# Kernel optimization log

Measured on AMD Instinct MI355X. Metric: run time of the kernel, lower is better.

The kernel has to match this reference:

```python
import jax, jax.numpy as jnp
import numpy as np

B, T, DIM, H, L = 16, 4096, 256, 128, 3  # hidden = dim // 2, 3 bidirectional layers


def setup_inputs() -> dict:
    key = jax.random.key(0)
    kx, ki, kh, kb = jax.random.split(key, 4)
    x = jax.random.normal(kx, (B, T, DIM), dtype=jnp.float32)
    # stacked params: [layer, direction(0=fwd,1=bwd), ...]; gates packed as (r, z, n)
    Wi = jax.random.normal(ki, (L, 2, DIM, 3 * H), dtype=jnp.float32) / np.sqrt(DIM).astype(np.float32)
    Wh = jax.random.normal(kh, (L, 2, H, 3 * H), dtype=jnp.float32) / np.sqrt(H).astype(np.float32)
    bh = jax.random.normal(kb, (L, 2, 3 * H), dtype=jnp.float32) * 0.01
    return {"x": x, "Wi": Wi, "Wh": Wh, "bh": bh}


def _gru_dir(x, Wi, Wh, bh, reverse):
    """Run a GRU over time; x [B,T,D] -> h sequence [B,T,H].

    flax nnx.GRUCell math: input denses have no bias, hidden denses have bias;
    n-gate hidden contribution (incl. its bias) is gated by r.
    """
    # precompute all input-side gate projections in one big GEMM (efficient)
    xg = jnp.einsum('btd,dk->btk', x, Wi)  # [B,T,3H]
    Whr, Whz, Whn = jnp.split(Wh, 3, axis=1)
    bhr, bhz, bhn = jnp.split(bh, 3)

    def step(h, xg_t):
        xr, xz, xn = jnp.split(xg_t, 3, axis=-1)
        r = jax.nn.sigmoid(xr + h @ Whr + bhr)
        z = jax.nn.sigmoid(xz + h @ Whz + bhz)
        n = jnp.tanh(xn + r * (h @ Whn + bhn))
        h_new = (1.0 - z) * n + z * h
        return h_new, h_new

    h0 = jnp.zeros((x.shape[0], Whr.shape[0]), x.dtype)
    _, ys = jax.lax.scan(step, h0, jnp.swapaxes(xg, 0, 1), reverse=reverse)
    return jnp.swapaxes(ys, 0, 1)  # [B,T,H], time-aligned with input (keep_order)


def reference(x, Wi, Wh, bh):
    n_layers = Wi.shape[0]
    for l in range(n_layers):
        fwd = _gru_dir(x, Wi[l, 0], Wh[l, 0], bh[l, 0], reverse=False)
        bwd = _gru_dir(x, Wi[l, 1], Wh[l, 1], bh[l, 1], reverse=True)
        x = jnp.concatenate([fwd, bwd], axis=-1)  # [B,T,2H]=[B,T,DIM]
    return x
```

## Files before the change

kernel.cpp:

```cpp
#include <hip/hip_runtime.h>

#define BB 16
#define TT 4096
#define DD 256
#define HH 128
#define G3 384
#define MM (BB*TT)

typedef unsigned short u16;
typedef unsigned int u32;
typedef __attribute__((ext_vector_type(8))) short short8;
typedef __attribute__((ext_vector_type(4))) float f32x4;
typedef __attribute__((ext_vector_type(2))) unsigned int u32x2;
typedef __attribute__((ext_vector_type(4))) unsigned int u32x4;

__device__ __forceinline__ float bf2f(u16 u) {
    return __uint_as_float(((u32)u) << 16);
}
__device__ __forceinline__ u16 f2bf(float f) {
    u32 u = __float_as_uint(f);
    u32 lsb = (u >> 16) & 1u;
    u += 0x7fffu + lsb;
    return (u16)(u >> 16);
}

__device__ __forceinline__ u32 cvt_pk2(float x, float y) {
    u32 pk;
    asm("v_cvt_pk_bf16_f32 %0, %1, %2" : "=v"(pk) : "v"(x), "v"(y));
    return pk;
}
__device__ __forceinline__ u32 cvt_bf16(float f) {
    u32 pk;
    asm("v_cvt_pk_bf16_f32 %0, %1, %2" : "=v"(pk) : "v"(f), "v"(f));
    return pk;
}
__device__ __forceinline__ void cvt2_hilo(float x, float y, u32& hi, u32& lo) {
    u32 h = cvt_pk2(x, y);
    float rx = x - __uint_as_float(h << 16);
    float ry = y - __uint_as_float(h & 0xffff0000u);
    hi = h;
    lo = cvt_pk2(rx, ry);
}

#define GBM 128
#define GBN 128
#define GBK 32
#define APAD 40

__global__ __launch_bounds__(256, 2) void gemm_in(const float* __restrict__ X,
                                                  const float* __restrict__ Wi,
                                                  float* __restrict__ XG) {
    __shared__ __align__(16) u16 Ahi[GBM][APAD];
    __shared__ __align__(16) u16 Alo[GBM][APAD];
    __shared__ __align__(16) u16 Bhi[GBN][APAD];
    __shared__ __align__(16) u16 Blo[GBN][APAD];

    const int tid = threadIdx.x;
    const int m0  = blockIdx.y * GBM;
    const int gc0 = blockIdx.x * GBN;
    const int dir = (gc0 >= G3) ? 1 : 0;
    const int n0  = gc0 - dir * G3;
    const float* Wd = Wi + (size_t)dir * DD * G3;

    const int lane = tid & 63;
    const int wv   = tid >> 6;
    const int wr   = wv >> 1;
    const int wc   = wv & 1;
    const int q    = lane >> 4;
    const int c    = lane & 15;

    f32x4 acc[4][4];
    #pragma unroll
    for (int i = 0; i < 4; ++i)
        #pragma unroll
        for (int j = 0; j < 4; ++j) acc[i][j] = (f32x4){0.f, 0.f, 0.f, 0.f};

    const int bn  = tid & 127;
    const int bkh = (tid >> 7) * 16;

    for (int k0 = 0; k0 < DD; k0 += GBK) {
        #pragma unroll
        for (int p = 0; p < 4; ++p) {
            int idx = tid + p * 256;
            int row = idx >> 3;
            int k4  = (idx & 7) * 4;
            float4 v = *(const float4*)(X + (size_t)(m0 + row) * DD + k0 + k4);
            u32 h01, l01, h23, l23;
            cvt2_hilo(v.x, v.y, h01, l01);
            cvt2_hilo(v.z, v.w, h23, l23);
            *(u32x2*)(&Ahi[row][k4]) = (u32x2){h01, h23};
            *(u32x2*)(&Alo[row][k4]) = (u32x2){l01, l23};
        }
        {
            float bv[16];
            #pragma unroll
            for (int j = 0; j < 16; ++j)
                bv[j] = Wd[(size_t)(k0 + bkh + j) * G3 + n0 + bn];
            u32 h[8], l[8];
            #pragma unroll
            for (int j = 0; j < 8; ++j)
                cvt2_hilo(bv[2 * j], bv[2 * j + 1], h[j], l[j]);
            *(u32x4*)(&Bhi[bn][bkh + 0]) = (u32x4){h[0], h[1], h[2], h[3]};
            *(u32x4*)(&Bhi[bn][bkh + 8]) = (u32x4){h[4], h[5], h[6], h[7]};
            *(u32x4*)(&Blo[bn][bkh + 0]) = (u32x4){l[0], l[1], l[2], l[3]};
            *(u32x4*)(&Blo[bn][bkh + 8]) = (u32x4){l[4], l[5], l[6], l[7]};
        }
        __syncthreads();
        short8 afh[4], afl[4], bfh[4], bfl[4];
        #pragma unroll
        for (int i = 0; i < 4; ++i) {
            afh[i] = *(const short8*)(&Ahi[wr * 64 + i * 16 + c][q * 8]);
            afl[i] = *(const short8*)(&Alo[wr * 64 + i * 16 + c][q * 8]);
            bfh[i] = *(const short8*)(&Bhi[wc * 64 + i * 16 + c][q * 8]);
            bfl[i] = *(const short8*)(&Blo[wc * 64 + i * 16 + c][q * 8]);
        }
        #pragma unroll
        for (int i = 0; i < 4; ++i)
            #pragma unroll
            for (int j = 0; j < 4; ++j) {
                acc[i][j] = __builtin_amdgcn_mfma_f32_16x16x32_bf16(afh[i], bfh[j], acc[i][j], 0, 0, 0);
                acc[i][j] = __builtin_amdgcn_mfma_f32_16x16x32_bf16(afh[i], bfl[j], acc[i][j], 0, 0, 0);
                acc[i][j] = __builtin_amdgcn_mfma_f32_16x16x32_bf16(afl[i], bfh[j], acc[i][j], 0, 0, 0);
            }
        __syncthreads();
    }
    #pragma unroll
    for (int i = 0; i < 4; ++i) {
        #pragma unroll
        for (int j = 0; j < 4; ++j) {
            const int n = n0 + wc * 64 + j * 16 + c;
            #pragma unroll
            for (int r = 0; r < 4; ++r) {
                const int m = m0 + wr * 64 + i * 16 + q * 4 + r;
                XG[((size_t)dir * MM + m) * G3 + n] = acc[i][j][r];
            }
        }
    }
}

__device__ __forceinline__ float fast_sigmoid(float x) {
    float e = __expf(-x);
    return __builtin_amdgcn_rcpf(1.f + e);
}
__device__ __forceinline__ float fast_tanh(float x) {
    float e = __expf(2.f * x);
    return 1.f - 2.f * __builtin_amdgcn_rcpf(1.f + e);
}

__device__ __forceinline__ float permswap_add(float g) {
    u32 gu = __float_as_uint(g);
    u32x2 r = __builtin_amdgcn_permlane32_swap(gu, gu, false, false);
    return __uint_as_float(r[0]) + __uint_as_float(r[1]);
}

struct XG3 { float r, z, n; };
__device__ __forceinline__ XG3 load3(const float* p) {
    XG3 v;
    v.r = p[0];
    v.z = p[128];
    v.n = p[256];
    return v;
}

#define HLO_OFF (2 * HH + 32)

__global__ __launch_bounds__(512, 1) void gru_rec(const float* __restrict__ XG,
                                                  const float* __restrict__ Wh,
                                                  const float* __restrict__ bh,
                                                  float* __restrict__ Xout) {
    const int wg   = blockIdx.x;
    const int dir  = wg & 1;
    const int b    = wg >> 1;
    const int tid  = threadIdx.x;
    const int lane = tid & 63;
    const int wave = tid >> 6;
    const int q    = lane >> 4;
    const int c    = lane & 15;
    const int hcol = wave * 16 + c;

    __shared__ __align__(16) u16 hbuf[HLO_OFF + 2 * HH];

    short8 bfr[3][4];
    {
        const float* W = Wh + (size_t)dir * HH * G3;
        #pragma unroll
        for (int g = 0; g < 3; ++g) {
            const int n = g * 128 + hcol;
            #pragma unroll
            for (int ch = 0; ch < 4; ++ch) {
                short8 vh;
                #pragma unroll
                for (int j = 0; j < 8; ++j) {
                    int k = ch * 32 + q * 8 + j;
                    vh[j] = (short)f2bf(W[(size_t)k * G3 + n]);
                }
                bfr[g][ch] = vh;
            }
        }
    }
    float hb[3];
    #pragma unroll
    for (int g = 0; g < 3; ++g) hb[g] = 0.5f * bh[dir * G3 + g * 128 + hcol];

    short8 a[4];
    #pragma unroll
    for (int ch = 0; ch < 4; ++ch)
        #pragma unroll
        for (int j = 0; j < 8; ++j) a[ch][j] = 0;
    float ho = 0.f;

    f32x4 accR = {0.f, 0.f, 0.f, 0.f};
    f32x4 accZ = {0.f, 0.f, 0.f, 0.f};
    f32x4 accN = {0.f, 0.f, 0.f, 0.f};

    const int t0    = dir ? (TT - 1) : 0;
    const int gstep = dir ? -G3 : G3;
    const int ostep = dir ? -DD : DD;

    const float* xp = XG + ((size_t)dir * MM + (size_t)b * TT + t0) * G3 + hcol;
    float* op = Xout + ((size_t)b * TT + t0) * DD + dir * HH + hcol;

    const u16* hrd = hbuf + ((c < 8) ? 0 : HLO_OFF) + q * 8;
    u16* hw_hi = hbuf + hcol;
    u16* hw_lo = hbuf + HLO_OFF + hcol;

    XG3 x0 = load3(xp);
    XG3 x1 = load3(xp + gstep);
    XG3 x2 = load3(xp + 2 * gstep);
    XG3 x3 = load3(xp + 3 * gstep);
    const float* xpf = xp + 4 * gstep;

#define SUBSTEP(S, XV, PK)                                                     \
    {                                                                          \
            \
        float xr = XV.r, xz = XV.z, xn = XV.n;                                 \
        if (t + (S) + 4 < TT) { XV = load3(xpf + (PK) * gstep); }              \
                  \
        accR[0] = __builtin_fmaf(0.5f, xr, hb[0]);                             \
        accZ[0] = __builtin_fmaf(0.5f, xz, hb[1]);                             \
        accN[0] = hb[2];                                                       \
                                   \
        _Pragma("unroll")                                                      \
        for (int ch = 0; ch < 4; ++ch) {                                       \
            accR = __builtin_amdgcn_mfma_f32_16x16x32_bf16(a[ch], bfr[0][ch], accR, 0, 0, 0); \
            accZ = __builtin_amdgcn_mfma_f32_16x16x32_bf16(a[ch], bfr[1][ch], accZ, 0, 0, 0); \
            accN = __builtin_amdgcn_mfma_f32_16x16x32_bf16(a[ch], bfr[2][ch], accN, 0, 0, 0); \
        }                                                                      \
        float pr = permswap_add(accR[0]);                                      \
        float pz = permswap_add(accZ[0]);                                      \
        float pm = permswap_add(accN[0]);                                      \
        float rg = fast_sigmoid(pr);                                           \
        float zg = fast_sigmoid(pz);                                           \
        float ng = fast_tanh(xn + rg * pm);                                    \
        float hn = (1.f - zg) * ng + zg * ho;                                  \
        ho = hn;                                                               \
                                 \
        u32 pk_hi = cvt_bf16(hn);                                              \
        float lo_f = hn - __uint_as_float(pk_hi << 16);                        \
        u32 pk_lo = cvt_bf16(lo_f);                                            \
        const int pb = ((S) + 1) & 1;                                          \
        if (q == 0) {                                                          \
            op[(S) * ostep] = hn;                                              \
            hw_hi[pb * HH]  = (u16)pk_hi;                                      \
        } else if (q == 1) {                                                   \
            hw_lo[pb * HH]  = (u16)pk_lo;                                      \
        }                                                                      \
        asm volatile("s_waitcnt lgkmcnt(0)\n\ts_barrier" ::: "memory");        \
        if (t + (S) + 1 < TT) {                                                \
            a[0] = *(const short8*)(hrd + pb * HH + 0);                        \
            a[1] = *(const short8*)(hrd + pb * HH + 32);                       \
            a[2] = *(const short8*)(hrd + pb * HH + 64);                       \
            a[3] = *(const short8*)(hrd + pb * HH + 96);                       \
        }                                                                      \
    }

    for (int t = 0; t < TT; t += 4) {
        SUBSTEP(0, x0, 0)
        SUBSTEP(1, x1, 1)
        xpf += 2 * gstep;
        SUBSTEP(2, x2, 0)
        SUBSTEP(3, x3, 1)
        xpf += 2 * gstep;
        op += 4 * ostep;
    }
#undef SUBSTEP
}

extern "C" void kernel_launch(void* const* d_in, const int* in_sizes, int n_in,
                              void* d_out, int out_size, void* d_ws, size_t ws_size,
                              hipStream_t stream) {
    const float* x  = (const float*)d_in[0];
    const float* Wi = (const float*)d_in[1];
    const float* Wh = (const float*)d_in[2];
    const float* bh = (const float*)d_in[3];
    float* out = (float*)d_out;

    float* XG = (float*)d_ws;

    for (int l = 0; l < 3; ++l) {
        const float* in  = (l == 0) ? x : out;
        const float* Wil = Wi + (size_t)l * 2 * DD * G3;
        const float* Whl = Wh + (size_t)l * 2 * HH * G3;
        const float* bhl = bh + (size_t)l * 2 * G3;

        gemm_in<<<dim3(6, MM / GBM), 256, 0, stream>>>(in, Wil, XG);
        gru_rec<<<32, 512, 0, stream>>>(XG, Whl, bhl, out);
    }
}
```

Before: 5.667 ms.

## Halve recurrent workgroup to 4 waves, each computing two 16-column tiles

```diff
diff --git a/kernel.cpp b/kernel.cpp
--- a/kernel.cpp
+++ b/kernel.cpp
@@ -153,18 +153,18 @@
     return __uint_as_float(r[0]) + __uint_as_float(r[1]);
 }
 
-struct XG3 { float r, z, n; };
-__device__ __forceinline__ XG3 load3(const float* p) {
-    XG3 v;
-    v.r = p[0];
-    v.z = p[128];
-    v.n = p[256];
+struct XG6 { float r0, r1, z0, z1, n0, n1; };
+__device__ __forceinline__ XG6 load6(const float* p) {
+    XG6 v;
+    v.r0 = p[0];   v.r1 = p[16];
+    v.z0 = p[128]; v.z1 = p[144];
+    v.n0 = p[256]; v.n1 = p[272];
     return v;
 }
 
 #define HLO_OFF (2 * HH + 32)
 
-__global__ __launch_bounds__(512, 1) void gru_rec(const float* __restrict__ XG,
+__global__ __launch_bounds__(256, 1) void gru_rec(const float* __restrict__ XG,
                                                   const float* __restrict__ Wh,
                                                   const float* __restrict__ bh,
                                                   float* __restrict__ Xout) {
@@ -176,94 +176,124 @@
     const int wave = tid >> 6;
     const int q    = lane >> 4;
     const int c    = lane & 15;
-    const int hcol = wave * 16 + c;
+    const int col0 = wave * 32 + c;
 
     __shared__ __align__(16) u16 hbuf[HLO_OFF + 2 * HH];
 
-    short8 bfr[3][4];
+    short8 bfr[3][2][4];
     {
         const float* W = Wh + (size_t)dir * HH * G3;
         #pragma unroll
-        for (int g = 0; g < 3; ++g) {
-            const int n = g * 128 + hcol;
-            #pragma unroll
-            for (int ch = 0; ch < 4; ++ch) {
-                short8 vh;
+        for (int g = 0; g < 3; ++g)
+            #pragma unroll
+            for (int ti = 0; ti < 2; ++ti) {
+                const int n = g * 128 + wave * 32 + ti * 16 + c;
                 #pragma unroll
-                for (int j = 0; j < 8; ++j) {
-                    int k = ch * 32 + q * 8 + j;
-                    vh[j] = (short)f2bf(W[(size_t)k * G3 + n]);
+                for (int ch = 0; ch < 4; ++ch) {
+                    short8 vh;
+                    #pragma unroll
+                    for (int j = 0; j < 8; ++j) {
+                        int k = ch * 32 + q * 8 + j;
+                        vh[j] = (short)f2bf(W[(size_t)k * G3 + n]);
+                    }
+                    bfr[g][ti][ch] = vh;
                 }
-                bfr[g][ch] = vh;
             }
-        }
-    }
-    float hb[3];
+    }
+    float hb[3][2];
     #pragma unroll
-    for (int g = 0; g < 3; ++g) hb[g] = 0.5f * bh[dir * G3 + g * 128 + hcol];
+    for (int g = 0; g < 3; ++g)
+        #pragma unroll
+        for (int ti = 0; ti < 2; ++ti)
+            hb[g][ti] = 0.5f * bh[dir * G3 + g * 128 + wave * 32 + ti * 16 + c];
 
     short8 a[4];
     #pragma unroll
     for (int ch = 0; ch < 4; ++ch)
         #pragma unroll
         for (int j = 0; j < 8; ++j) a[ch][j] = 0;
-    float ho = 0.f;
-
-    f32x4 accR = {0.f, 0.f, 0.f, 0.f};
-    f32x4 accZ = {0.f, 0.f, 0.f, 0.f};
-    f32x4 accN = {0.f, 0.f, 0.f, 0.f};
+    float ho0 = 0.f, ho1 = 0.f;
+
+    f32x4 aR0 = {0,0,0,0}, aZ0 = {0,0,0,0}, aN0 = {0,0,0,0};
+    f32x4 aR1 = {0,0,0,0}, aZ1 = {0,0,0,0}, aN1 = {0,0,0,0};
 
     const int t0    = dir ? (TT - 1) : 0;
     const int gstep = dir ? -G3 : G3;
     const int ostep = dir ? -DD : DD;
 
-    const float* xp = XG + ((size_t)dir * MM + (size_t)b * TT + t0) * G3 + hcol;
-    float* op = Xout + ((size_t)b * TT + t0) * DD + dir * HH + hcol;
+    const float* xp = XG + ((size_t)dir * MM + (size_t)b * TT + t0) * G3 + col0;
+    float* op = Xout + ((size_t)b * TT + t0) * DD + dir * HH + col0;
 
     const u16* hrd = hbuf + ((c < 8) ? 0 : HLO_OFF) + q * 8;
-    u16* hw_hi = hbuf + hcol;
-    u16* hw_lo = hbuf + HLO_OFF + hcol;
-
-    XG3 x0 = load3(xp);
-    XG3 x1 = load3(xp + gstep);
-    XG3 x2 = load3(xp + 2 * gstep);
-    XG3 x3 = load3(xp + 3 * gstep);
+    u16* hw_hi = hbuf + col0;
+    u16* hw_lo = hbuf + HLO_OFF + col0;
+
+    XG6 x0 = load6(xp);
+    XG6 x1 = load6(xp + gstep);
+    XG6 x2 = load6(xp + 2 * gstep);
+    XG6 x3 = load6(xp + 3 * gstep);
     const float* xpf = xp + 4 * gstep;
 
 #define SUBSTEP(S, XV, PK)                                                     \
     {                                                                          \
             \
-        float xr = XV.r, xz = XV.z, xn = XV.n;                                 \
-        if (t + (S) + 4 < TT) { XV = load3(xpf + (PK) * gstep); }              \
+        float xr0 = XV.r0, xr1 = XV.r1, xz0 = XV.z0, xz1 = XV.z1;              \
+        float xn0 = XV.n0, xn1 = XV.n1;                                        \
+        if (t + (S) + 4 < TT) { XV = load6(xpf + (PK) * gstep); }              \
                   \
-        accR[0] = __builtin_fmaf(0.5f, xr, hb[0]);                             \
-        accZ[0] = __builtin_fmaf(0.5f, xz, hb[1]);                             \
-        accN[0] = hb[2];                                                       \
-                                   \
+        aR0[0] = __builtin_fmaf(0.5f, xr0, hb[0][0]);                          \
+        aZ0[0] = __builtin_fmaf(0.5f, xz0, hb[1][0]);                          \
+        aN0[0] = hb[2][0];                                                     \
+        aR1[0] = __builtin_fmaf(0.5f, xr1, hb[0][1]);                          \
+        aZ1[0] = __builtin_fmaf(0.5f, xz1, hb[1][1]);                          \
+        aN1[0] = hb[2][1];                                                     \
+                       \
         _Pragma("unroll")                                                      \
         for (int ch = 0; ch < 4; ++ch) {                                       \
-            accR = __builtin_amdgcn_mfma_f32_16x16x32_bf16(a[ch], bfr[0][ch], accR, 0, 0, 0); \
-            accZ = __builtin_amdgcn_mfma_f32_16x16x32_bf16(a[ch], bfr[1][ch], accZ, 0, 0, 0); \
-            accN = __builtin_amdgcn_mfma_f32_16x16x32_bf16(a[ch], bfr[2][ch], accN, 0, 0, 0); \
-        }                                                                      \
-        float pr = permswap_add(accR[0]);                                      \
-        float pz = permswap_add(accZ[0]);                                      \
-        float pm = permswap_add(accN[0]);                                      \
-        float rg = fast_sigmoid(pr);                                           \
-        float zg = fast_sigmoid(pz);                                           \
-        float ng = fast_tanh(xn + rg * pm);                                    \
-        float hn = (1.f - zg) * ng + zg * ho;                                  \
-        ho = hn;                                                               \
-                                 \
-        u32 pk_hi = cvt_bf16(hn);                                              \
-        float lo_f = hn - __uint_as_float(pk_hi << 16);                        \
-        u32 pk_lo = cvt_bf16(lo_f);                                            \
+            aR0 = __builtin_amdgcn_mfma_f32_16x16x32_bf16(a[ch], bfr[0][0][ch], aR0, 0, 0, 0); \
+            aZ0 = __builtin_amdgcn_mfma_f32_16x16x32_bf16(a[ch], bfr[1][0][ch], aZ0, 0, 0, 0); \
+            aN0 = __builtin_amdgcn_mfma_f32_16x16x32_bf16(a[ch], bfr[2][0][ch], aN0, 0, 0, 0); \
+            aR1 = __builtin_amdgcn_mfma_f32_16x16x32_bf16(a[ch], bfr[0][1][ch], aR1, 0, 0, 0); \
+            aZ1 = __builtin_amdgcn_mfma_f32_16x16x32_bf16(a[ch], bfr[1][1][ch], aZ1, 0, 0, 0); \
+            aN1 = __builtin_amdgcn_mfma_f32_16x16x32_bf16(a[ch], bfr[2][1][ch], aN1, 0, 0, 0); \
+        }                                                                      \
+        float hn0, hn1;                                                        \
+        {                                                                      \
+            float pr = permswap_add(aR0[0]);                                   \
+            float pz = permswap_add(aZ0[0]);                                   \
+            float pm = permswap_add(aN0[0]);                                   \
+            float rg = fast_sigmoid(pr);                                       \
+            float zg = fast_sigmoid(pz);                                       \
+            float ng = fast_tanh(xn0 + rg * pm);                               \
+            hn0 = (1.f - zg) * ng + zg * ho0;                                  \
+            ho0 = hn0;                                                         \
+        }                                                                      \
+        {                                                                      \
+            float pr = permswap_add(aR1[0]);                                   \
+            float pz = permswap_add(aZ1[0]);                                   \
+            float pm = permswap_add(aN1[0]);                                   \
+            float rg = fast_sigmoid(pr);                                       \
+            float zg = fast_sigmoid(pz);                                       \
+            float ng = fast_tanh(xn1 + rg * pm);                               \
+            hn1 = (1.f - zg) * ng + zg * ho1;                                  \
+            ho1 = hn1;                                                         \
+        }                                                                      \
+                                             \
+        u32 pk_hi0 = cvt_bf16(hn0);                                            \
+        u32 pk_hi1 = cvt_bf16(hn1);                                            \
+        float lo_f0 = hn0 - __uint_as_float(pk_hi0 << 16);                     \
+        float lo_f1 = hn1 - __uint_as_float(pk_hi1 << 16);                     \
+        u32 pk_lo0 = cvt_bf16(lo_f0);                                          \
+        u32 pk_lo1 = cvt_bf16(lo_f1);                                          \
         const int pb = ((S) + 1) & 1;                                          \
         if (q == 0) {                                                          \
-            op[(S) * ostep] = hn;                                              \
-            hw_hi[pb * HH]  = (u16)pk_hi;                                      \
+            op[(S) * ostep]      = hn0;                                        \
+            op[(S) * ostep + 16] = hn1;                                        \
+            hw_hi[pb * HH]      = (u16)pk_hi0;                                 \
+            hw_hi[pb * HH + 16] = (u16)pk_hi1;                                 \
         } else if (q == 1) {                                                   \
-            hw_lo[pb * HH]  = (u16)pk_lo;                                      \
+            hw_lo[pb * HH]      = (u16)pk_lo0;                                 \
+            hw_lo[pb * HH + 16] = (u16)pk_lo1;                                 \
         }                                                                      \
         asm volatile("s_waitcnt lgkmcnt(0)\n\ts_barrier" ::: "memory");        \
         if (t + (S) + 1 < TT) {                                                \
@@ -304,6 +334,6 @@
         const float* bhl = bh + (size_t)l * 2 * G3;
 
         gemm_in<<<dim3(6, MM / GBM), 256, 0, stream>>>(in, Wil, XG);
-        gru_rec<<<32, 512, 0, stream>>>(XG, Whl, bhl, out);
-    }
-}
+        gru_rec<<<32, 256, 0, stream>>>(XG, Whl, bhl, out);
+    }
+}
```

New measurement: 7.183 ms. 1.27x slower.
